# Optimization experiments

Measured on AMD Instinct MI355X. Metric: run time of the kernel, lower is better.

## Reference

```python
import jax, jax.numpy as jnp
import numpy as np

NUM_NODES = 50000
NUM_HYPEREDGES = 10000
NUM_INCIDENCES = 800000
CHANNELS = 256
NEG_SLOPE = 0.01  # torch leaky_relu default negative_slope


def setup_inputs() -> dict:
    key = jax.random.key(0)
    k_n, k_e, k_emb, k_cw, k_lw, k_lb = jax.random.split(key, 6)
    node_idx = jax.random.randint(k_n, (NUM_INCIDENCES,), 0, NUM_NODES, dtype=jnp.int32)
    edge_idx = jax.random.randint(k_e, (NUM_INCIDENCES,), 0, NUM_HYPEREDGES, dtype=jnp.int32)
    edge_index = jnp.stack([node_idx, edge_idx], axis=0)  # [2, nnz] incidence list
    s = 1.0 / np.sqrt(CHANNELS).astype(np.float32)
    emb = jax.random.normal(k_emb, (NUM_NODES, CHANNELS), jnp.float32)  # Node2Vec embedding table
    conv_w = jax.random.normal(k_cw, (CHANNELS, CHANNELS), jnp.float32) * s  # HypergraphConv.lin (no bias)
    conv_b = jnp.zeros((CHANNELS,), jnp.float32)  # HypergraphConv.bias
    lin_w = jax.random.normal(k_lw, (CHANNELS, CHANNELS), jnp.float32) * s
    lin_b = jax.random.normal(k_lb, (CHANNELS,), jnp.float32) * s
    return {"emb": emb, "conv_w": conv_w, "conv_b": conv_b,
            "lin_w": lin_w, "lin_b": lin_b, "edge_index": edge_index}


def reference(emb, conv_w, conv_b, lin_w, lin_b, edge_index):
    node_idx, edge_idx = edge_index[0], edge_index[1]
    # HypergraphConv (use_attention=False): X' = D^-1 H B^-1 H^T (X W^T) + b
    x = emb @ conv_w.T  # [N, C]
    ones = jnp.ones((NUM_INCIDENCES,), x.dtype)
    D = jax.ops.segment_sum(ones, node_idx, num_segments=NUM_NODES)       # node degree
    Dinv = jnp.where(D > 0, 1.0 / D, 0.0)
    B = jax.ops.segment_sum(ones, edge_idx, num_segments=NUM_HYPEREDGES)  # hyperedge degree
    Binv = jnp.where(B > 0, 1.0 / B, 0.0)
    # node -> hyperedge aggregation
    e = jax.ops.segment_sum(x[node_idx], edge_idx, num_segments=NUM_HYPEREDGES) * Binv[:, None]  # [E, C]
    # hyperedge -> node aggregation
    n = jax.ops.segment_sum(e[edge_idx], node_idx, num_segments=NUM_NODES) * Dinv[:, None] + conv_b  # [N, C]
    y = jax.nn.leaky_relu(n, NEG_SLOPE)
    g = y.T @ y  # [C, C] Gram
    out = jax.nn.leaky_relu(g @ lin_w.T + lin_b, NEG_SLOPE)
    return out
```

## Files before the change

### kernel.cpp

```cpp
#include <hip/hip_runtime.h>

#define N_NODES 50000
#define N_EDGES 10000
#define NNZ     800000
#define C       256
#define SLOPE   0.01f
#define KTOT    50176
#define KCHUNK  512
#define NZB     98
#define MPAD    10048

#define NB      250
#define EB_E    40
#define EB_N    200
#define CHUNK   3125
#define CAP     6000

#define EAGG_G  628
#define NAGG_G  784

#define OFF_CC_E    0
#define OFF_CC_N    1024
#define OFF_CUR_E   2048
#define OFF_CUR_N   3072
#define ZERO_BYTES  4096
#define OFF_CB_E    266240
#define OFF_CB_N    267264
#define OFF_RS_N    268288
#define OFF_RS_E    468480
#define OFF_BUF_E   508672
#define OFF_BUF_N   3708672
#define OFF_CSR_E   6908672
#define OFF_CSR_N   10108672
#define OFF_EMBH    13308672
#define OFF_YT      13308672
#define OFF_EACC    39000064
#define OFF_E2      44144640
#define OFF_CWH     49289216
#define OFF_PART    49420288

typedef __attribute__((ext_vector_type(8))) short short8;
typedef __attribute__((ext_vector_type(4))) float floatx4;

static __device__ __forceinline__ unsigned short f2bf(float f) {
    unsigned int u = __float_as_uint(f);
    u = (u + 0x7fffu + ((u >> 16) & 1u)) >> 16;
    return (unsigned short)u;
}

static __device__ __forceinline__ void acc_bf8(const uint4 d, float* a) {
    a[0] += __uint_as_float(d.x << 16);
    a[1] += __uint_as_float(d.x & 0xffff0000u);
    a[2] += __uint_as_float(d.y << 16);
    a[3] += __uint_as_float(d.y & 0xffff0000u);
    a[4] += __uint_as_float(d.z << 16);
    a[5] += __uint_as_float(d.z & 0xffff0000u);
    a[6] += __uint_as_float(d.w << 16);
    a[7] += __uint_as_float(d.w & 0xffff0000u);
}

static __device__ __forceinline__ void idx8(const uint4 pk, int* ix) {
    ix[0] = (int)(pk.x & 0xffffu); ix[1] = (int)(pk.x >> 16);
    ix[2] = (int)(pk.y & 0xffffu); ix[3] = (int)(pk.y >> 16);
    ix[4] = (int)(pk.z & 0xffffu); ix[5] = (int)(pk.z >> 16);
    ix[6] = (int)(pk.w & 0xffffu); ix[7] = (int)(pk.w >> 16);
}

__global__ __launch_bounds__(256) void zero_kernel(float4* __restrict__ p, int n4) {
    int i = blockIdx.x * 256 + threadIdx.x;
    if (i < n4) p[i] = make_float4(0.f, 0.f, 0.f, 0.f);
}

#define PREP_EMB_BLOCKS 6251
#define PREP_CW_BLOCKS  32
__global__ __launch_bounds__(256) void prep_kernel(const float4* __restrict__ emb4,
                                                   uint4* __restrict__ embh4,
                                                   const float4* __restrict__ cw4,
                                                   uint4* __restrict__ cwh4,
                                                   const int* __restrict__ node_idx,
                                                   const int* __restrict__ edge_idx,
                                                   int* __restrict__ cc_e,
                                                   int* __restrict__ cc_n) {
    __shared__ int he[NB], hn[NB];
    int b = blockIdx.x, tid = threadIdx.x;
    if (b < PREP_EMB_BLOCKS) {
        int i = b * 256 + tid;
        if (i >= 1600032) return;
        uint4 o = {0u, 0u, 0u, 0u};
        if (i < 1600000) {
            float4 f0 = emb4[2 * i], f1 = emb4[2 * i + 1];
            o.x = f2bf(f0.x) | ((unsigned)f2bf(f0.y) << 16);
            o.y = f2bf(f0.z) | ((unsigned)f2bf(f0.w) << 16);
            o.z = f2bf(f1.x) | ((unsigned)f2bf(f1.y) << 16);
            o.w = f2bf(f1.z) | ((unsigned)f2bf(f1.w) << 16);
        }
        int node = i >> 5, c = i & 31;
        embh4[(size_t)(((c >> 2) * 50001 + node) << 2) + (c & 3)] = o;
    } else if (b < PREP_EMB_BLOCKS + PREP_CW_BLOCKS) {
        int i = (b - PREP_EMB_BLOCKS) * 256 + tid;
        float4 f0 = cw4[2 * i], f1 = cw4[2 * i + 1];
        uint4 o;
        o.x = f2bf(f0.x) | ((unsigned)f2bf(f0.y) << 16);
        o.y = f2bf(f0.z) | ((unsigned)f2bf(f0.w) << 16);
        o.z = f2bf(f1.x) | ((unsigned)f2bf(f1.y) << 16);
        o.w = f2bf(f1.z) | ((unsigned)f2bf(f1.w) << 16);
        cwh4[i] = o;
    } else {
        int base = (b - PREP_EMB_BLOCKS - PREP_CW_BLOCKS) * CHUNK;
        for (int i = tid; i < NB; i += 256) { he[i] = 0; hn[i] = 0; }
        __syncthreads();
        for (int i = tid; i < CHUNK; i += 256) {
            atomicAdd(&he[edge_idx[base + i] / EB_E], 1);
            atomicAdd(&hn[node_idx[base + i] / EB_N], 1);
        }
        __syncthreads();
        for (int k = tid; k < NB; k += 256) {
            if (he[k]) atomicAdd(&cc_e[k], he[k]);
            if (hn[k]) atomicAdd(&cc_n[k], hn[k]);
        }
    }
}

__global__ __launch_bounds__(256) void coarse_scan_kernel(const int* __restrict__ cc_e,
                                                          const int* __restrict__ cc_n,
                                                          int* __restrict__ cb_e,
                                                          int* __restrict__ cb_n) {
    __shared__ int tmp[256];
    int tid = threadIdx.x;
    int v = (tid < NB) ? cc_e[tid] : 0;
    tmp[tid] = v;
    __syncthreads();
    for (int off = 1; off < 256; off <<= 1) {
        int t = (tid >= off) ? tmp[tid - off] : 0;
        __syncthreads();
        tmp[tid] += t;
        __syncthreads();
    }
    if (tid < NB) cb_e[tid + 1] = tmp[tid];
    if (tid == 0) cb_e[0] = 0;
    __syncthreads();
    v = (tid < NB) ? cc_n[tid] : 0;
    tmp[tid] = v;
    __syncthreads();
    for (int off = 1; off < 256; off <<= 1) {
        int t = (tid >= off) ? tmp[tid - off] : 0;
        __syncthreads();
        tmp[tid] += t;
        __syncthreads();
    }
    if (tid < NB) cb_n[tid + 1] = tmp[tid];
    if (tid == 0) cb_n[0] = 0;
}

__global__ __launch_bounds__(256) void bucket_scatter_kernel(const int* __restrict__ node_idx,
                                                             const int* __restrict__ edge_idx,
                                                             const int* __restrict__ cb_e,
                                                             const int* __restrict__ cb_n,
                                                             int* __restrict__ cur_e,
                                                             int* __restrict__ cur_n,
                                                             int* __restrict__ buf_e,
                                                             int* __restrict__ buf_n) {
    __shared__ int he[NB], hn[NB], be[NB], bn[NB];
    int tid = threadIdx.x;
    int base = blockIdx.x * CHUNK;
    for (int i = tid; i < NB; i += 256) { he[i] = 0; hn[i] = 0; }
    __syncthreads();
    int pe[13], pn[13];
    #pragma unroll
    for (int k = 0; k < 13; k++) {
        int i = tid + k * 256;
        if (i < CHUNK) {
            int e = edge_idx[base + i], v = node_idx[base + i];
            int ke = e / EB_E, kn = v / EB_N;
            pe[k] = (ke << 12) | atomicAdd(&he[ke], 1);
            pn[k] = (kn << 12) | atomicAdd(&hn[kn], 1);
        }
    }
    __syncthreads();
    for (int k = tid; k < NB; k += 256) {
        int c = he[k];
        be[k] = cb_e[k] + (c ? atomicAdd(&cur_e[k], c) : 0);
        int cn = hn[k];
        bn[k] = cb_n[k] + (cn ? atomicAdd(&cur_n[k], cn) : 0);
    }
    __syncthreads();
    #pragma unroll
    for (int k = 0; k < 13; k++) {
        int i = tid + k * 256;
        if (i < CHUNK) {
            int e = edge_idx[base + i], v = node_idx[base + i];
            int ke = pe[k] >> 12, oe = pe[k] & 4095;
            buf_e[be[ke] + oe] = (v << 6) | (e - ke * EB_E);
            int kn = pn[k] >> 12, on = pn[k] & 4095;
            buf_n[bn[kn] + on] = (e << 8) | (v - kn * EB_N);
        }
    }
}

__global__ __launch_bounds__(256) void bucket_sort_kernel(const int* __restrict__ buf_e,
                                                          const int* __restrict__ buf_n,
                                                          const int* __restrict__ cb_e,
                                                          const int* __restrict__ cb_n,
                                                          unsigned short* __restrict__ csr_e,
                                                          unsigned short* __restrict__ csr_n,
                                                          int* __restrict__ rs_e,
                                                          int* __restrict__ rs_n) {
    __shared__ int A[CAP];
    __shared__ int h[EB_N], bs[EB_N];
    int tid = threadIdx.x;
    bool edgeSide = blockIdx.x < NB;
    int k = edgeSide ? blockIdx.x : blockIdx.x - NB;
    int eb = edgeSide ? EB_E : EB_N;
    int shift = edgeSide ? 6 : 8;
    int mask = (1 << shift) - 1;
    const int* cb  = edgeSide ? cb_e : cb_n;
    const int* buf = edgeSide ? buf_e : buf_n;
    unsigned short* csr = edgeSide ? csr_e : csr_n;
    int* rs        = edgeSide ? rs_e : rs_n;
    int base = cb[k];
    int cnt = cb[k + 1] - base;
    for (int i = tid; i < eb; i += 256) h[i] = 0;
    __syncthreads();
    for (int i = tid; i < cnt; i += 256) {
        int it = buf[base + i];
        if (i < CAP) A[i] = it;
        atomicAdd(&h[it & mask], 1);
    }
    __syncthreads();
    if (tid == 0) {
        int s = 0;
        for (int j = 0; j < eb; j++) { bs[j] = s; s += h[j]; }
    }
    __syncthreads();
    for (int j = tid; j < eb; j += 256) {
        rs[k * eb + j] = base + bs[j];
        h[j] = 0;
    }
    if (tid == 0 && k == NB - 1) rs[edgeSide ? N_EDGES : N_NODES] = NNZ;
    __syncthreads();
    for (int i = tid; i < cnt; i += 256) {
        int it = (i < CAP) ? A[i] : buf[base + i];
        int loc = it & mask;
        int off = bs[loc] + atomicAdd(&h[loc], 1);
        csr[base + off] = (unsigned short)(it >> shift);
    }
}

__global__ __launch_bounds__(256) void edge_aggregate_kernel(const uint4* __restrict__ embh4,
                                                             const unsigned short* __restrict__ csr_e,
                                                             const int* __restrict__ rs_e,
                                                             unsigned short* __restrict__ e_acc_h) {
    int sid = blockIdx.x & 7, g = blockIdx.x >> 3;
    const uint4* __restrict__ tbl = embh4 + (size_t)sid * 50001 * 4;
    const uint4* __restrict__ csr4 = (const uint4*)csr_e;
    int tid = threadIdx.x;
    int w = tid >> 6, lane = tid & 63;
    int grp = lane >> 4, q = (lane >> 2) & 3, c4 = lane & 3;
    int ebase = g * 16 + w * 4;
    int rsv = rs_e[min(ebase + lane, N_EDGES)];
    int e = ebase + grp;
    int s = __shfl(rsv, grp), t = __shfl(rsv, grp + 1);
    float a[8] = {0.f, 0.f, 0.f, 0.f, 0.f, 0.f, 0.f, 0.f};
    for (int c = (s >> 3) + q; c * 8 < t; c += 4) {
        uint4 pk = csr4[c];
        int cb = c << 3;
        int ix[8];
        idx8(pk, ix);
        #pragma unroll
        for (int j = 0; j < 8; j++) {
            int i = cb + j;
            int r = (i >= s && i < t) ? ix[j] : N_NODES;
            acc_bf8(tbl[r * 4 + c4], a);
        }
    }
    #pragma unroll
    for (int off = 4; off <= 8; off <<= 1) {
        #pragma unroll
        for (int jj = 0; jj < 8; jj++) a[jj] += __shfl_xor(a[jj], off);
    }
    if (q == 0) {
        uint4 o;
        o.x = f2bf(a[0]) | ((unsigned)f2bf(a[1]) << 16);
        o.y = f2bf(a[2]) | ((unsigned)f2bf(a[3]) << 16);
        o.z = f2bf(a[4]) | ((unsigned)f2bf(a[5]) << 16);
        o.w = f2bf(a[6]) | ((unsigned)f2bf(a[7]) << 16);
        ((uint4*)(e_acc_h + (size_t)e * C + sid * 32))[c4] = o;
    }
}

__global__ __launch_bounds__(256) void edge_gemm_mfma_kernel(const unsigned short* __restrict__ e_acc_h,
                                                             const unsigned short* __restrict__ cwh,
                                                             const int* __restrict__ rs_e,
                                                             unsigned short* __restrict__ e2h) {
    __shared__ __align__(16) unsigned short As[64 * 72];
    __shared__ __align__(16) unsigned short Bs[64 * 72];
    int i0 = blockIdx.x * 64, j0 = blockIdx.y * 64;
    int tid = threadIdx.x;
    int w = tid >> 6, lane = tid & 63;
    int col = lane & 15, quad = lane >> 4;
    floatx4 acc[4] = {};
    for (int step = 0; step < 4; step++) {
        int kb = step * 64;
        __syncthreads();
        #pragma unroll
        for (int l = 0; l < 2; l++) {
            int slot = tid + l * 256;
            int row = slot >> 3, grp = slot & 7;
            uint4 da = *(const uint4*)(e_acc_h + (size_t)(i0 + row) * C + kb + grp * 8);
            *(uint4*)(&As[row * 72 + grp * 8]) = da;
            uint4 db = *(const uint4*)(cwh + (size_t)(j0 + row) * C + kb + grp * 8);
            *(uint4*)(&Bs[row * 72 + grp * 8]) = db;
        }
        __syncthreads();
        #pragma unroll
        for (int sub = 0; sub < 2; sub++) {
            short8 a = *(const short8*)(&As[(w * 16 + col) * 72 + sub * 32 + quad * 8]);
            #pragma unroll
            for (int jt = 0; jt < 4; jt++) {
                short8 b = *(const short8*)(&Bs[(jt * 16 + col) * 72 + sub * 32 + quad * 8]);
                acc[jt] = __builtin_amdgcn_mfma_f32_16x16x32_bf16(a, b, acc[jt], 0, 0, 0);
            }
        }
    }
    #pragma unroll
    for (int r = 0; r < 4; r++) {
        int m = i0 + w * 16 + quad * 4 + r;
        int deg = (m < N_EDGES) ? rs_e[m + 1] - rs_e[m] : 0;
        float binv = (deg > 0) ? 1.0f / (float)deg : 0.0f;
        #pragma unroll
        for (int jt = 0; jt < 4; jt++) {
            int ch = j0 + jt * 16 + col;
            e2h[(size_t)((ch >> 5) * MPAD + m) * 32 + (ch & 31)] = f2bf(acc[jt][r] * binv);
        }
    }
}

__global__ __launch_bounds__(256) void node_aggregate_t_kernel(const uint4* __restrict__ e2h4,
                                                               const unsigned short* __restrict__ csr_n,
                                                               const int* __restrict__ rs_n,
                                                               const float* __restrict__ conv_b,
                                                               unsigned short* __restrict__ yT) {
    __shared__ unsigned short T[32][66];
    int sid = blockIdx.x & 7, g = blockIdx.x >> 3;
    const uint4* __restrict__ tbl = e2h4 + (size_t)sid * MPAD * 4;
    const uint4* __restrict__ csr4 = (const uint4*)csr_n;
    int tid = threadIdx.x;
    int w = tid >> 6, lane = tid & 63;
    int q = lane >> 2, c4 = lane & 3;
    int n = g * 64 + w * 16 + q;
    int s = 0, t = 0;
    if (n < N_NODES) { s = rs_n[n]; t = rs_n[n + 1]; }
    float4 b0 = ((const float4*)conv_b)[sid * 8 + c4 * 2];
    float4 b1 = ((const float4*)conv_b)[sid * 8 + c4 * 2 + 1];
    float a[8] = {0.f, 0.f, 0.f, 0.f, 0.f, 0.f, 0.f, 0.f};
    for (int c = s >> 3; c * 8 < t; c++) {
        uint4 pk = csr4[c];
        int cb = c << 3;
        int ix[8];
        idx8(pk, ix);
        #pragma unroll
        for (int j = 0; j < 8; j++) {
            int i = cb + j;
            int r = (i >= s && i < t) ? ix[j] : N_EDGES;
            acc_bf8(tbl[r * 4 + c4], a);
        }
    }
    float dinv = (t > s) ? 1.0f / (float)(t - s) : 0.0f;
    float bb[8] = {b0.x, b0.y, b0.z, b0.w, b1.x, b1.y, b1.z, b1.w};
    #pragma unroll
    for (int jj = 0; jj < 8; jj++) {
        float r = a[jj] * dinv + bb[jj];
        r = (r > 0.f) ? r : SLOPE * r;
        if (n >= N_NODES) r = 0.f;
        T[c4 * 8 + jj][w * 16 + q] = f2bf(r);
    }
    __syncthreads();
    int rr = tid >> 3, cc = tid & 7;
    uint4 o;
    o.x = T[rr][cc * 8 + 0] | ((unsigned)T[rr][cc * 8 + 1] << 16);
    o.y = T[rr][cc * 8 + 2] | ((unsigned)T[rr][cc * 8 + 3] << 16);
    o.z = T[rr][cc * 8 + 4] | ((unsigned)T[rr][cc * 8 + 5] << 16);
    o.w = T[rr][cc * 8 + 6] | ((unsigned)T[rr][cc * 8 + 7] << 16);
    *(uint4*)(yT + (size_t)(sid * 32 + rr) * KTOT + g * 64 + cc * 8) = o;
}

__global__ __launch_bounds__(256) void gram_mfma_kernel(const unsigned short* __restrict__ yT,
                                                        float* __restrict__ part) {
    static const int PI[10] = {0, 0, 0, 0, 1, 1, 1, 2, 2, 3};
    static const int PJ[10] = {0, 1, 2, 3, 1, 2, 3, 2, 3, 3};
    __shared__ __align__(16) unsigned short As[64 * 72];
    __shared__ __align__(16) unsigned short Bs[64 * 72];
    int i0 = PI[blockIdx.x] * 64, j0 = PJ[blockIdx.x] * 64;
    bool diag = (i0 == j0);
    int kb0 = blockIdx.y * KCHUNK;
    int tid = threadIdx.x;
    int w = tid >> 6, lane = tid & 63;
    int col = lane & 15, quad = lane >> 4;
    floatx4 acc[4] = {};
    for (int step = 0; step < KCHUNK / 64; step++) {
        int kb = kb0 + step * 64;
        __syncthreads();
        #pragma unroll
        for (int l = 0; l < 2; l++) {
            int slot = tid + l * 256;
            int row = slot >> 3, grp = slot & 7;
            uint4 da = *(const uint4*)(yT + (size_t)(i0 + row) * KTOT + kb + grp * 8);
            *(uint4*)(&As[row * 72 + grp * 8]) = da;
            if (!diag) {
                uint4 db = *(const uint4*)(yT + (size_t)(j0 + row) * KTOT + kb + grp * 8);
                *(uint4*)(&Bs[row * 72 + grp * 8]) = db;
            }
        }
        __syncthreads();
        const unsigned short* Bb = diag ? As : Bs;
        #pragma unroll
        for (int sub = 0; sub < 2; sub++) {
            short8 a = *(const short8*)(&As[(w * 16 + col) * 72 + sub * 32 + quad * 8]);
            #pragma unroll
            for (int jt = 0; jt < 4; jt++) {
                short8 b = *(const short8*)(&Bb[(jt * 16 + col) * 72 + sub * 32 + quad * 8]);
                acc[jt] = __builtin_amdgcn_mfma_f32_16x16x32_bf16(a, b, acc[jt], 0, 0, 0);
            }
        }
    }
    float* slab = part + ((size_t)blockIdx.y * 10 + blockIdx.x) * 4096;
    #pragma unroll
    for (int jt = 0; jt < 4; jt++)
        #pragma unroll
        for (int r = 0; r < 4; r++)
            slab[(w * 16 + quad * 4 + r) * 64 + jt * 16 + col] = acc[jt][r];
}

__global__ __launch_bounds__(256) void greduce_out_kernel(const float* __restrict__ part,
                                                          const float* __restrict__ lin_w,
                                                          const float* __restrict__ lin_b,
                                                          float* __restrict__ out) {
    __shared__ float gs[C];
    int i = blockIdx.x, j = threadIdx.x;
    int a = i >> 6, b = j >> 6;
    int lo = min(a, b), hi = max(a, b);
    int t = lo * (7 - lo) / 2 + hi;
    int li = (a <= b) ? (i & 63) : (j & 63);
    int lj = (a <= b) ? (j & 63) : (i & 63);
    const float* p = part + (size_t)t * 4096 + li * 64 + lj;
    float s = 0.f;
    for (int z = 0; z < NZB; z++) s += p[(size_t)z * 40960];
    gs[j] = s;
    __syncthreads();
    float acc = lin_b[j];
    const float* wrow = lin_w + (size_t)j * C;
    for (int k = 0; k < C; k++) acc += gs[k] * wrow[k];
    out[(size_t)i * C + j] = (acc > 0.f) ? acc : SLOPE * acc;
}

extern "C" void kernel_launch(void* const* d_in, const int* in_sizes, int n_in,
                              void* d_out, int out_size, void* d_ws, size_t ws_size,
                              hipStream_t stream) {
    const float* emb    = (const float*)d_in[0];
    const float* conv_w = (const float*)d_in[1];
    const float* conv_b = (const float*)d_in[2];
    const float* lin_w  = (const float*)d_in[3];
    const float* lin_b  = (const float*)d_in[4];
    const int*   eidx   = (const int*)d_in[5];
    const int* node_idx = eidx;
    const int* edge_idx = eidx + NNZ;

    char* ws = (char*)d_ws;
    int* cc_e  = (int*)(ws + OFF_CC_E);
    int* cc_n  = (int*)(ws + OFF_CC_N);
    int* cur_e = (int*)(ws + OFF_CUR_E);
    int* cur_n = (int*)(ws + OFF_CUR_N);
    int* cb_e  = (int*)(ws + OFF_CB_E);
    int* cb_n  = (int*)(ws + OFF_CB_N);
    int* rs_n  = (int*)(ws + OFF_RS_N);
    int* rs_e  = (int*)(ws + OFF_RS_E);
    int* buf_e = (int*)(ws + OFF_BUF_E);
    int* buf_n = (int*)(ws + OFF_BUF_N);
    unsigned short* csr_e = (unsigned short*)(ws + OFF_CSR_E);
    unsigned short* csr_n = (unsigned short*)(ws + OFF_CSR_N);
    uint4* embh4 = (uint4*)(ws + OFF_EMBH);
    unsigned short* e_acc_h = (unsigned short*)(ws + OFF_EACC);
    unsigned short* e2h = (unsigned short*)(ws + OFF_E2);
    unsigned short* cwh = (unsigned short*)(ws + OFF_CWH);
    unsigned short* yT  = (unsigned short*)(ws + OFF_YT);
    float* part = (float*)(ws + OFF_PART);
    float* out = (float*)d_out;

    zero_kernel<<<1, 256, 0, stream>>>((float4*)ws, ZERO_BYTES / 16);

    prep_kernel<<<PREP_EMB_BLOCKS + PREP_CW_BLOCKS + 256, 256, 0, stream>>>(
        (const float4*)emb, embh4, (const float4*)conv_w, (uint4*)cwh,
        node_idx, edge_idx, cc_e, cc_n);

    coarse_scan_kernel<<<1, 256, 0, stream>>>(cc_e, cc_n, cb_e, cb_n);

    bucket_scatter_kernel<<<256, 256, 0, stream>>>(node_idx, edge_idx, cb_e, cb_n,
                                                   cur_e, cur_n, buf_e, buf_n);

    bucket_sort_kernel<<<2 * NB, 256, 0, stream>>>(buf_e, buf_n, cb_e, cb_n,
                                                   csr_e, csr_n, rs_e, rs_n);

    edge_aggregate_kernel<<<8 * EAGG_G, 256, 0, stream>>>(embh4, csr_e, rs_e, e_acc_h);

    edge_gemm_mfma_kernel<<<dim3(MPAD / 64, C / 64), 256, 0, stream>>>(e_acc_h, cwh, rs_e, e2h);

    node_aggregate_t_kernel<<<8 * NAGG_G, 256, 0, stream>>>((const uint4*)e2h, csr_n, rs_n,
                                                            conv_b, yT);

    gram_mfma_kernel<<<dim3(10, NZB), 256, 0, stream>>>(yT, part);

    greduce_out_kernel<<<C, 256, 0, stream>>>(part, lin_w, lin_b, out);
}
```

Measured before the change: 269.1 us.

## Pad CSR segments to multiples of eight with sentinel entries

The bucket sort now lays out each edge's and each node's CSR segment at an 8-aligned offset and fills the padding with a sentinel index that points at the zero row. It also writes per-segment degrees into a newly zeroed array. Both aggregation kernels can then walk whole uint4 index chunks without per-element range checks and without touching chunks shared with neighbouring segments. In exchange the CSR buffers grow, the zero kernel clears more memory, and the sort does extra sentinel writes.

```diff
diff --git a/kernel.cpp b/kernel.cpp
--- a/kernel.cpp
+++ b/kernel.cpp
@@ -15,6 +15,8 @@
 #define EB_N    200
 #define CHUNK   3125
 #define CAP     6000
+#define MP_E    288
+#define MP_N    1408
 
 #define EAGG_G  628
 #define NAGG_G  784
@@ -23,7 +25,9 @@
 #define OFF_CC_N    1024
 #define OFF_CUR_E   2048
 #define OFF_CUR_N   3072
-#define ZERO_BYTES  4096
+#define OFF_DEG_E   4096
+#define OFF_DEG_N   45056
+#define ZERO_BYTES  245760
 #define OFF_CB_E    266240
 #define OFF_CB_N    267264
 #define OFF_RS_N    268288
@@ -204,20 +208,26 @@
                                                           unsigned short* __restrict__ csr_e,
                                                           unsigned short* __restrict__ csr_n,
                                                           int* __restrict__ rs_e,
-                                                          int* __restrict__ rs_n) {
+                                                          int* __restrict__ rs_n,
+                                                          int* __restrict__ deg_e,
+                                                          int* __restrict__ deg_n) {
     __shared__ int A[CAP];
-    __shared__ int h[EB_N], bs[EB_N];
+    __shared__ int h[EB_N], bs[EB_N], cs[EB_N];
     int tid = threadIdx.x;
     bool edgeSide = blockIdx.x < NB;
     int k = edgeSide ? blockIdx.x : blockIdx.x - NB;
     int eb = edgeSide ? EB_E : EB_N;
     int shift = edgeSide ? 6 : 8;
     int mask = (1 << shift) - 1;
+    int mp = edgeSide ? MP_E : MP_N;
+    int sent = edgeSide ? N_NODES : N_EDGES;
     const int* cb  = edgeSide ? cb_e : cb_n;
     const int* buf = edgeSide ? buf_e : buf_n;
     unsigned short* csr = edgeSide ? csr_e : csr_n;
-    int* rs        = edgeSide ? rs_e : rs_n;
+    int* rs  = edgeSide ? rs_e : rs_n;
+    int* deg = edgeSide ? deg_e : deg_n;
     int base = cb[k];
+    int base_pad = (base + k * mp + 7) & ~7;
     int cnt = cb[k + 1] - base;
     for (int i = tid; i < eb; i += 256) h[i] = 0;
     __syncthreads();
@@ -229,26 +239,33 @@
     __syncthreads();
     if (tid == 0) {
         int s = 0;
-        for (int j = 0; j < eb; j++) { bs[j] = s; s += h[j]; }
+        for (int j = 0; j < eb; j++) { bs[j] = s; s += (h[j] + 7) & ~7; }
     }
     __syncthreads();
     for (int j = tid; j < eb; j += 256) {
-        rs[k * eb + j] = base + bs[j];
+        rs[k * eb + j] = base_pad + bs[j];
+        deg[k * eb + j] = h[j];
+        cs[j] = h[j];
         h[j] = 0;
     }
     if (tid == 0 && k == NB - 1) rs[edgeSide ? N_EDGES : N_NODES] = NNZ;
     __syncthreads();
+    for (int j = tid; j < eb; j += 256) {
+        int c0 = cs[j], e0 = (c0 + 7) & ~7;
+        for (int x = c0; x < e0; x++) csr[base_pad + bs[j] + x] = (unsigned short)sent;
+    }
     for (int i = tid; i < cnt; i += 256) {
         int it = (i < CAP) ? A[i] : buf[base + i];
         int loc = it & mask;
         int off = bs[loc] + atomicAdd(&h[loc], 1);
-        csr[base + off] = (unsigned short)(it >> shift);
+        csr[base_pad + off] = (unsigned short)(it >> shift);
     }
 }
 
 __global__ __launch_bounds__(256) void edge_aggregate_kernel(const uint4* __restrict__ embh4,
                                                              const unsigned short* __restrict__ csr_e,
                                                              const int* __restrict__ rs_e,
+                                                             const int* __restrict__ deg_e,
                                                              unsigned short* __restrict__ e_acc_h) {
     int sid = blockIdx.x & 7, g = blockIdx.x >> 3;
     const uint4* __restrict__ tbl = embh4 + (size_t)sid * 50001 * 4;
@@ -256,22 +273,17 @@
     int tid = threadIdx.x;
     int w = tid >> 6, lane = tid & 63;
     int grp = lane >> 4, q = (lane >> 2) & 3, c4 = lane & 3;
-    int ebase = g * 16 + w * 4;
-    int rsv = rs_e[min(ebase + lane, N_EDGES)];
-    int e = ebase + grp;
-    int s = __shfl(rsv, grp), t = __shfl(rsv, grp + 1);
+    int e = g * 16 + w * 4 + grp;
+    int s = rs_e[e];
+    int dg = deg_e[e];
+    int c0 = s >> 3, nc = (dg + 7) >> 3;
     float a[8] = {0.f, 0.f, 0.f, 0.f, 0.f, 0.f, 0.f, 0.f};
-    for (int c = (s >> 3) + q; c * 8 < t; c += 4) {
+    for (int c = c0 + q; c < c0 + nc; c += 4) {
         uint4 pk = csr4[c];
-        int cb = c << 3;
         int ix[8];
         idx8(pk, ix);
         #pragma unroll
-        for (int j = 0; j < 8; j++) {
-            int i = cb + j;
-            int r = (i >= s && i < t) ? ix[j] : N_NODES;
-            acc_bf8(tbl[r * 4 + c4], a);
-        }
+        for (int j = 0; j < 8; j++) acc_bf8(tbl[ix[j] * 4 + c4], a);
     }
     #pragma unroll
     for (int off = 4; off <= 8; off <<= 1) {
@@ -290,7 +302,7 @@
 
 __global__ __launch_bounds__(256) void edge_gemm_mfma_kernel(const unsigned short* __restrict__ e_acc_h,
                                                              const unsigned short* __restrict__ cwh,
-                                                             const int* __restrict__ rs_e,
+                                                             const int* __restrict__ deg_e,
                                                              unsigned short* __restrict__ e2h) {
     __shared__ __align__(16) unsigned short As[64 * 72];
     __shared__ __align__(16) unsigned short Bs[64 * 72];
@@ -325,8 +337,8 @@
     #pragma unroll
     for (int r = 0; r < 4; r++) {
         int m = i0 + w * 16 + quad * 4 + r;
-        int deg = (m < N_EDGES) ? rs_e[m + 1] - rs_e[m] : 0;
-        float binv = (deg > 0) ? 1.0f / (float)deg : 0.0f;
+        int dg = deg_e[m];
+        float binv = (dg > 0) ? 1.0f / (float)dg : 0.0f;
         #pragma unroll
         for (int jt = 0; jt < 4; jt++) {
             int ch = j0 + jt * 16 + col;
@@ -338,6 +350,7 @@
 __global__ __launch_bounds__(256) void node_aggregate_t_kernel(const uint4* __restrict__ e2h4,
                                                                const unsigned short* __restrict__ csr_n,
                                                                const int* __restrict__ rs_n,
+                                                               const int* __restrict__ deg_n,
                                                                const float* __restrict__ conv_b,
                                                                unsigned short* __restrict__ yT) {
     __shared__ unsigned short T[32][66];
@@ -348,24 +361,20 @@
     int w = tid >> 6, lane = tid & 63;
     int q = lane >> 2, c4 = lane & 3;
     int n = g * 64 + w * 16 + q;
-    int s = 0, t = 0;
-    if (n < N_NODES) { s = rs_n[n]; t = rs_n[n + 1]; }
+    int s = rs_n[min(n, N_NODES)];
+    int dg = deg_n[n];
+    int c0 = s >> 3, nc = (dg + 7) >> 3;
     float4 b0 = ((const float4*)conv_b)[sid * 8 + c4 * 2];
     float4 b1 = ((const float4*)conv_b)[sid * 8 + c4 * 2 + 1];
     float a[8] = {0.f, 0.f, 0.f, 0.f, 0.f, 0.f, 0.f, 0.f};
-    for (int c = s >> 3; c * 8 < t; c++) {
+    for (int c = c0; c < c0 + nc; c++) {
         uint4 pk = csr4[c];
-        int cb = c << 3;
         int ix[8];
         idx8(pk, ix);
         #pragma unroll
-        for (int j = 0; j < 8; j++) {
-            int i = cb + j;
-            int r = (i >= s && i < t) ? ix[j] : N_EDGES;
-            acc_bf8(tbl[r * 4 + c4], a);
-        }
-    }
-    float dinv = (t > s) ? 1.0f / (float)(t - s) : 0.0f;
+        for (int j = 0; j < 8; j++) acc_bf8(tbl[ix[j] * 4 + c4], a);
+    }
+    float dinv = (dg > 0) ? 1.0f / (float)dg : 0.0f;
     float bb[8] = {b0.x, b0.y, b0.z, b0.w, b1.x, b1.y, b1.z, b1.w};
     #pragma unroll
     for (int jj = 0; jj < 8; jj++) {
@@ -470,6 +479,8 @@
     int* cc_n  = (int*)(ws + OFF_CC_N);
     int* cur_e = (int*)(ws + OFF_CUR_E);
     int* cur_n = (int*)(ws + OFF_CUR_N);
+    int* deg_e = (int*)(ws + OFF_DEG_E);
+    int* deg_n = (int*)(ws + OFF_DEG_N);
     int* cb_e  = (int*)(ws + OFF_CB_E);
     int* cb_n  = (int*)(ws + OFF_CB_N);
     int* rs_n  = (int*)(ws + OFF_RS_N);
@@ -486,7 +497,7 @@
     float* part = (float*)(ws + OFF_PART);
     float* out = (float*)d_out;
 
-    zero_kernel<<<1, 256, 0, stream>>>((float4*)ws, ZERO_BYTES / 16);
+    zero_kernel<<<ZERO_BYTES / 4096, 256, 0, stream>>>((float4*)ws, ZERO_BYTES / 16);
 
     prep_kernel<<<PREP_EMB_BLOCKS + PREP_CW_BLOCKS + 256, 256, 0, stream>>>(
         (const float4*)emb, embh4, (const float4*)conv_w, (uint4*)cwh,
@@ -498,14 +509,15 @@
                                                    cur_e, cur_n, buf_e, buf_n);
 
     bucket_sort_kernel<<<2 * NB, 256, 0, stream>>>(buf_e, buf_n, cb_e, cb_n,
-                                                   csr_e, csr_n, rs_e, rs_n);
-
-    edge_aggregate_kernel<<<8 * EAGG_G, 256, 0, stream>>>(embh4, csr_e, rs_e, e_acc_h);
-
-    edge_gemm_mfma_kernel<<<dim3(MPAD / 64, C / 64), 256, 0, stream>>>(e_acc_h, cwh, rs_e, e2h);
+                                                   csr_e, csr_n, rs_e, rs_n,
+                                                   deg_e, deg_n);
+
+    edge_aggregate_kernel<<<8 * EAGG_G, 256, 0, stream>>>(embh4, csr_e, rs_e, deg_e, e_acc_h);
+
+    edge_gemm_mfma_kernel<<<dim3(MPAD / 64, C / 64), 256, 0, stream>>>(e_acc_h, cwh, deg_e, e2h);
 
     node_aggregate_t_kernel<<<8 * NAGG_G, 256, 0, stream>>>((const uint4*)e2h, csr_n, rs_n,
-                                                            conv_b, yT);
+                                                            deg_n, conv_b, yT);
 
     gram_mfma_kernel<<<dim3(10, NZB), 256, 0, stream>>>(yT, part);
 
```

Result: no change. 267.7 us (-0.5%).
